# Optimization experiments

Measured on AMD Instinct MI355X. Metric: run time of the kernel, lower is better.

## Reference

```python
import jax, jax.numpy as jnp
import numpy as np

B, S, I, H = 64, 2048, 512, 512


def setup_inputs() -> dict:
    key = jax.random.key(0)
    k1, k2, k3 = jax.random.split(key, 3)
    x_enc = jax.random.normal(k1, (B, S, I), dtype=jnp.float32)
    # Packed gate weights: columns = [i | f | o | c | d], scaled like typical init
    W = jax.random.normal(k2, (I + H, 5 * H), dtype=jnp.float32) * (1.0 / np.sqrt(I + H))
    b = jax.random.normal(k3, (5 * H,), dtype=jnp.float32) * 0.01
    return {"x_enc": x_enc, "W": W, "b": b}


def reference(x_enc, W, b):
    Bb, Ss, Ii = x_enc.shape
    Hh = W.shape[1] // 5

    def step(carry, x_t):
        h, c = carry
        z = jnp.concatenate([x_t, h], axis=-1) @ W + b  # [B, 5H]
        zi, zf, zo, zc, zd = jnp.split(z, 5, axis=-1)
        i_t = jax.nn.sigmoid(zi)
        f_t = jax.nn.sigmoid(zf)
        o_t = jax.nn.sigmoid(zo)
        c_prime = f_t * c + i_t * jnp.tanh(zc)
        d_t = jnp.tanh(zd)
        c_new = c_prime + d_t * (c_prime - c)  # highway-style update
        h_new = o_t * jnp.tanh(c_new)
        return (h_new, c_new), h_new

    h0 = jnp.zeros((Bb, Hh), dtype=x_enc.dtype)
    c0 = jnp.zeros((Bb, Hh), dtype=x_enc.dtype)
    xs = jnp.transpose(x_enc, (1, 0, 2))  # [S, B, I]
    _, ys = jax.lax.scan(step, (h0, c0), xs)
    return jnp.transpose(ys, (1, 0, 2))  # [B, S, H]
```

## Files before the change

kernel.cpp:

```cpp
#include <hip/hip_runtime.h>
#include <stdint.h>


typedef _Float16 h8 __attribute__((ext_vector_type(8)));
typedef _Float16 h4v __attribute__((ext_vector_type(4)));
typedef float f4 __attribute__((ext_vector_type(4)));

#define SCOPE_AGENT __HIP_MEMORY_SCOPE_AGENT

__device__ __forceinline__ float sigf(float x) {
  x = fminf(fmaxf(x, -40.f), 40.f);
  return 1.f / (1.f + __expf(-x));
}
__device__ __forceinline__ float tanh_f(float x) {
  x = fminf(fmaxf(x, -20.f), 20.f);
  const float e = __expf(2.f * x);
  return (e - 1.f) / (e + 1.f);
}

__global__ __launch_bounds__(256) void k_wt(const float* __restrict__ W,
                                            _Float16* __restrict__ Wt) {
  __shared__ __align__(16) _Float16 tl[64][68];
  const int bk = blockIdx.x & 15;
  const int bn = blockIdx.x >> 4;
  const int t = threadIdx.x;
  {
    const int r = t >> 2, c4 = t & 3;
    const float4* s4 = (const float4*)(W + (size_t)(bk * 64 + r) * 2560 + bn * 64 + c4 * 16);
#pragma unroll
    for (int i = 0; i < 4; i++) {
      float4 v = s4[i];
      tl[r][c4 * 16 + i * 4 + 0] = (_Float16)v.x;
      tl[r][c4 * 16 + i * 4 + 1] = (_Float16)v.y;
      tl[r][c4 * 16 + i * 4 + 2] = (_Float16)v.z;
      tl[r][c4 * 16 + i * 4 + 3] = (_Float16)v.w;
    }
  }
  __syncthreads();
  {
    const int nr = t >> 2, kk = (t & 3) * 16;
    h8 o0, o1;
#pragma unroll
    for (int i = 0; i < 8; i++) {
      o0[i] = tl[kk + i][nr];
      o1[i] = tl[kk + 8 + i][nr];
    }
    _Float16* dst = Wt + (size_t)(bn * 64 + nr) * 1024 + bk * 64 + kk;
    *(h8*)dst = o0;
    *(h8*)(dst + 8) = o1;
  }
}

__global__ __launch_bounds__(256) void k_zx(const float* __restrict__ X,
                                            const _Float16* __restrict__ Wt,
                                            const float* __restrict__ bias,
                                            _Float16* __restrict__ Zx,
                                            int s_base, int CS) {
  __shared__ __align__(16) _Float16 As[128][72];
  __shared__ __align__(16) _Float16 Bs[128][72];
  const int bid = blockIdx.x;
  const int nblk = bid % 20;
  const int mblk = bid / 20;
  const int tilesPerB = CS >> 7;
  const int b = mblk / tilesPerB;
  const int s0 = (mblk - b * tilesPerB) << 7;
  const int t = threadIdx.x;
  const int wid = t >> 6, lane = t & 63;
  const int wr = wid >> 1, wc = wid & 1;
  const int lr = (lane >> 4) * 4, lc = lane & 15;
  const int koff = (lane >> 4) * 8;

  const f4 zero4 = {0.f, 0.f, 0.f, 0.f};
  f4 acc[4][4];
#pragma unroll
  for (int i = 0; i < 4; i++)
#pragma unroll
    for (int j = 0; j < 4; j++) acc[i][j] = zero4;

  const float* Xb = X + ((size_t)b * 2048 + (size_t)(s_base + s0)) * 512;
  const _Float16* Bb = Wt + (size_t)nblk * 128 * 1024;
  const int rA = t >> 1, hf = t & 1;

  for (int k0 = 0; k0 < 512; k0 += 64) {
    const float4* s4 = (const float4*)(Xb + (size_t)rA * 512 + k0 + hf * 32);
#pragma unroll
    for (int i = 0; i < 8; i++) {
      float4 v = s4[i];
      h4v o = {(_Float16)v.x, (_Float16)v.y, (_Float16)v.z, (_Float16)v.w};
      *(h4v*)&As[rA][hf * 32 + i * 4] = o;
    }
    const h8* bs = (const h8*)(Bb + (size_t)rA * 1024 + k0 + hf * 32);
#pragma unroll
    for (int i = 0; i < 4; i++) *(h8*)&Bs[rA][hf * 32 + i * 8] = bs[i];
    __syncthreads();
#pragma unroll
    for (int kk = 0; kk < 2; kk++) {
      h8 af[4], bf[4];
      const int kr = kk * 32 + koff;
#pragma unroll
      for (int i = 0; i < 4; i++) af[i] = *(const h8*)&As[wr * 64 + i * 16 + lc][kr];
#pragma unroll
      for (int j = 0; j < 4; j++) bf[j] = *(const h8*)&Bs[wc * 64 + j * 16 + lc][kr];
#pragma unroll
      for (int i = 0; i < 4; i++)
#pragma unroll
        for (int j = 0; j < 4; j++)
          acc[i][j] = __builtin_amdgcn_mfma_f32_16x16x32_f16(af[i], bf[j], acc[i][j], 0, 0, 0);
    }
    __syncthreads();
  }
#pragma unroll
  for (int j = 0; j < 4; j++) {
    const int col = nblk * 128 + wc * 64 + j * 16 + lc;
    const float bc = bias[col];
#pragma unroll
    for (int i = 0; i < 4; i++) {
#pragma unroll
      for (int r = 0; r < 4; r++) {
        const int srow = s0 + wr * 64 + i * 16 + lr + r;
        Zx[((size_t)b * CS + srow) * 2560 + col] = (_Float16)(acc[i][j][r] + bc);
      }
    }
  }
}

__global__ __launch_bounds__(256) void k_rec(
    const _Float16* __restrict__ Zx, const _Float16* __restrict__ Wt,
    float* __restrict__ Y, uint32_t* __restrict__ hbuf,
    _Float16* __restrict__ hstate, float* __restrict__ cstate,
    uint32_t* __restrict__ flags, int s_base, int CS) {
  __shared__ __align__(16) _Float16 WsT[40][520];
  __shared__ __align__(16) _Float16 hs[16][520];
  __shared__ __align__(16) float zsh[16][40];
  __shared__ __align__(16) _Float16 zxs[16][40];
  __shared__ __align__(16) float cbuf[128];
  __shared__ __align__(16) uint16_t hn[128];

  const int bid = blockIdx.x;
  const int grp = bid >> 6, ci = bid & 63;
  const int tid = threadIdx.x;
  const int wid = tid >> 6, lane = tid & 63;
  const int hbase = ci * 8;

#pragma unroll
  for (int i = 0; i < 10; i++) {
    const int idx = i * 256 + tid;
    const int lcw = idx >> 6;
    const int ch = idx & 63;
    const int g = lcw >> 3, j = lcw & 7;
    const h8* src = (const h8*)(Wt + (size_t)(g * 512 + hbase + j) * 1024 + 512 + ch * 8);
    *(h8*)&WsT[lcw][ch * 8] = *src;
  }
  if (tid < 128) {
    cbuf[tid] = cstate[(grp * 64 + ci) * 128 + tid];
    const int m = tid >> 3, j = tid & 7;
    _Float16 hv = hstate[(size_t)(grp * 16 + m) * 512 + hbase + j];
    hn[tid] = *(const uint16_t*)&hv;
  }
  __syncthreads();
  if (wid == 0) {
    const int m = lane >> 2, q = lane & 3;
    const uint32_t v = ((const uint32_t*)hn)[lane];
    __hip_atomic_store(&hbuf[(size_t)((0 * 4 + grp) * 16 + m) * 256 + ci * 4 + q], v,
                       __ATOMIC_RELAXED, SCOPE_AGENT);
    asm volatile("s_waitcnt vmcnt(0)" ::: "memory");
    if (lane == 0)
      __hip_atomic_store(&flags[grp * 64 + ci], 1u, __ATOMIC_RELAXED, SCOPE_AGENT);
  }

  uint32_t* hs32 = (uint32_t*)&hs[0][0];

  for (int t = 0; t < CS; t++) {
    if (wid == 3) {
      for (int c = lane; c < 80; c += 64) {
        const int m = c / 5, g = c % 5;
        const h8* src =
            (const h8*)(Zx + ((size_t)(grp * 16 + m) * CS + t) * 2560 + g * 512 + hbase);
        *(h8*)&zxs[m][g * 8] = *src;
      }
    }
    if (wid == 0) {
      const uint32_t target = (uint32_t)(t + 1);
      while (true) {
        const uint32_t v =
            __hip_atomic_load(&flags[grp * 64 + lane], __ATOMIC_RELAXED, SCOPE_AGENT);
        if (__all((int)(v >= target))) break;
      }
    }
    __syncthreads();
    {
      const uint32_t* src = hbuf + (size_t)(((t & 1) * 4 + grp) * 16) * 256;
#pragma unroll
      for (int i = 0; i < 16; i++) {
        const uint32_t v =
            __hip_atomic_load(&src[i * 256 + tid], __ATOMIC_RELAXED, SCOPE_AGENT);
        hs32[i * 260 + tid] = v;
      }
    }
    __syncthreads();
    if (wid < 3) {
      f4 acc = {0.f, 0.f, 0.f, 0.f};
      const int nloc = wid * 16 + (lane & 15);
      const int wrow = nloc < 40 ? nloc : 39;
      const int koff = (lane >> 4) * 8;
#pragma unroll
      for (int ks = 0; ks < 16; ks++) {
        const h8 a = *(const h8*)&hs[lane & 15][ks * 32 + koff];
        const h8 bb = *(const h8*)&WsT[wrow][ks * 32 + koff];
        acc = __builtin_amdgcn_mfma_f32_16x16x32_f16(a, bb, acc, 0, 0, 0);
      }
      if (nloc < 40) {
        const int rb = (lane >> 4) * 4;
#pragma unroll
        for (int r = 0; r < 4; r++)
          zsh[rb + r][nloc] = acc[r] + (float)zxs[rb + r][nloc];
      }
    }
    __syncthreads();
    if (tid < 128) {
      const int m = tid >> 3, j = tid & 7;
      const float zi = zsh[m][j], zf = zsh[m][8 + j], zo = zsh[m][16 + j];
      const float zc = zsh[m][24 + j], zd = zsh[m][32 + j];
      const float ig = sigf(zi), fg = sigf(zf), og = sigf(zo);
      const float c0 = cbuf[tid];
      const float cp = fg * c0 + ig * tanh_f(zc);
      const float dg = tanh_f(zd);
      const float cn = cp + dg * (cp - c0);
      const float hv = og * tanh_f(cn);
      cbuf[tid] = cn;
      Y[((size_t)(grp * 16 + m) * 2048 + (size_t)(s_base + t)) * 512 + hbase + j] = hv;
      const _Float16 hfv = (_Float16)hv;
      hn[tid] = *(const uint16_t*)&hfv;
      if (t == CS - 1) {
        cstate[(grp * 64 + ci) * 128 + tid] = cn;
        hstate[(size_t)(grp * 16 + m) * 512 + hbase + j] = hfv;
      }
    }
    __syncthreads();
    if (wid == 0) {
      const int m = lane >> 2, q = lane & 3;
      const uint32_t v = ((const uint32_t*)hn)[lane];
      __hip_atomic_store(
          &hbuf[(size_t)((((t + 1) & 1) * 4 + grp) * 16 + m) * 256 + ci * 4 + q], v,
          __ATOMIC_RELAXED, SCOPE_AGENT);
      asm volatile("s_waitcnt vmcnt(0)" ::: "memory");
      if (lane == 0)
        __hip_atomic_store(&flags[grp * 64 + ci], (uint32_t)(t + 2), __ATOMIC_RELAXED,
                           SCOPE_AGENT);
    }
  }
}

extern "C" void kernel_launch(void* const* d_in, const int* in_sizes, int n_in,
                              void* d_out, int out_size, void* d_ws, size_t ws_size,
                              hipStream_t stream) {
  const float* X = (const float*)d_in[0];
  const float* W = (const float*)d_in[1];
  const float* bias = (const float*)d_in[2];
  float* Y = (float*)d_out;
  char* ws = (char*)d_ws;

  const size_t szWt = (size_t)2560 * 1024 * 2;
  int CS = 128;
  for (int c = 2048; c >= 128; c >>= 1) {
    const size_t need = szWt + (size_t)64 * c * 2560 * 2 + 400 * 1024;
    if (need <= ws_size) { CS = c; break; }
  }
  const size_t offZx = szWt;
  const size_t szZx = (size_t)64 * CS * 2560 * 2;
  const size_t offHbuf = offZx + szZx;
  const size_t szHbuf = (size_t)2 * 4 * 16 * 256 * 4;
  const size_t offHst = offHbuf + szHbuf;
  const size_t szHst = (size_t)4 * 16 * 512 * 2;
  const size_t offCst = offHst + szHst;
  const size_t szCst = (size_t)4 * 64 * 128 * 4;
  const size_t offFlg = offCst + szCst;
  const size_t szFlg = 256 * 4;

  _Float16* Wt = (_Float16*)(ws + 0);
  _Float16* Zx = (_Float16*)(ws + offZx);
  uint32_t* hbuf = (uint32_t*)(ws + offHbuf);
  _Float16* hstate = (_Float16*)(ws + offHst);
  float* cstate = (float*)(ws + offCst);
  uint32_t* flags = (uint32_t*)(ws + offFlg);

  k_wt<<<640, 256, 0, stream>>>(W, Wt);
  (void)hipMemsetAsync(ws + offHst, 0, szHst + szCst, stream);

  const int nch = 2048 / CS;
  for (int ch = 0; ch < nch; ch++) {
    const int sb = ch * CS;
    k_zx<<<CS * 10, 256, 0, stream>>>(X, Wt, bias, Zx, sb, CS);
    (void)hipMemsetAsync(ws + offFlg, 0, szFlg, stream);
    k_rec<<<256, 256, 0, stream>>>(Zx, Wt, Y, hbuf, hstate, cstate, flags, sb, CS);
  }
  (void)in_sizes; (void)n_in; (void)out_size;
}
```

Baseline: 15.76 ms.

## Replace flag-based step barrier with tagged per-element h exchange

The separate per-block flag array and its polling wave are removed. Each h element is now stored with a 16-bit step tag in the upper half of a 32-bit word, and consumers spin on the tags of the data they load directly. This removes the extra syncthreads, the s_waitcnt before flag stores, and the flag memset between chunks. It also permutes block-to-column mapping, likely to spread blocks across XCDs. The hbuf doubles in size, and each element is published individually with a relaxed atomic, so ordering correctness depends on the tag check alone.

```diff
diff --git a/kernel.cpp b/kernel.cpp
--- a/kernel.cpp
+++ b/kernel.cpp
@@ -128,16 +128,16 @@
     const _Float16* __restrict__ Zx, const _Float16* __restrict__ Wt,
     float* __restrict__ Y, uint32_t* __restrict__ hbuf,
     _Float16* __restrict__ hstate, float* __restrict__ cstate,
-    uint32_t* __restrict__ flags, int s_base, int CS) {
+    int s_base, int CS) {
   __shared__ __align__(16) _Float16 WsT[40][520];
   __shared__ __align__(16) _Float16 hs[16][520];
   __shared__ __align__(16) float zsh[16][40];
   __shared__ __align__(16) _Float16 zxs[16][40];
   __shared__ __align__(16) float cbuf[128];
-  __shared__ __align__(16) uint16_t hn[128];
 
   const int bid = blockIdx.x;
-  const int grp = bid >> 6, ci = bid & 63;
+  const int grp = bid >> 6;
+  const int ci = ((bid & 7) << 3) | ((bid >> 3) & 7);
   const int tid = threadIdx.x;
   const int wid = tid >> 6, lane = tid & 63;
   const int hbase = ci * 8;
@@ -155,22 +155,19 @@
     cbuf[tid] = cstate[(grp * 64 + ci) * 128 + tid];
     const int m = tid >> 3, j = tid & 7;
     _Float16 hv = hstate[(size_t)(grp * 16 + m) * 512 + hbase + j];
-    hn[tid] = *(const uint16_t*)&hv;
+    uint16_t hb;
+    __builtin_memcpy(&hb, &hv, 2);
+    const uint32_t v = ((uint32_t)(s_base + 1) << 16) | (uint32_t)hb;
+    __hip_atomic_store(&hbuf[((size_t)((s_base & 1) * 4 + grp) * 16 + m) * 512 + hbase + j],
+                       v, __ATOMIC_RELAXED, SCOPE_AGENT);
   }
   __syncthreads();
-  if (wid == 0) {
-    const int m = lane >> 2, q = lane & 3;
-    const uint32_t v = ((const uint32_t*)hn)[lane];
-    __hip_atomic_store(&hbuf[(size_t)((0 * 4 + grp) * 16 + m) * 256 + ci * 4 + q], v,
-                       __ATOMIC_RELAXED, SCOPE_AGENT);
-    asm volatile("s_waitcnt vmcnt(0)" ::: "memory");
-    if (lane == 0)
-      __hip_atomic_store(&flags[grp * 64 + ci], 1u, __ATOMIC_RELAXED, SCOPE_AGENT);
-  }
 
   uint32_t* hs32 = (uint32_t*)&hs[0][0];
 
   for (int t = 0; t < CS; t++) {
+    const int G = s_base + t;
+    const uint32_t tag = (uint32_t)(G + 1);
     if (wid == 3) {
       for (int c = lane; c < 80; c += 64) {
         const int m = c / 5, g = c % 5;
@@ -179,22 +176,20 @@
         *(h8*)&zxs[m][g * 8] = *src;
       }
     }
-    if (wid == 0) {
-      const uint32_t target = (uint32_t)(t + 1);
-      while (true) {
-        const uint32_t v =
-            __hip_atomic_load(&flags[grp * 64 + lane], __ATOMIC_RELAXED, SCOPE_AGENT);
-        if (__all((int)(v >= target))) break;
-      }
-    }
-    __syncthreads();
     {
-      const uint32_t* src = hbuf + (size_t)(((t & 1) * 4 + grp) * 16) * 256;
+      const uint64_t* src =
+          (const uint64_t*)(hbuf + (size_t)((G & 1) * 4 + grp) * 16 * 512);
+      uint64_t w[16];
+#pragma unroll
+      for (int i = 0; i < 16; i++)
+        w[i] = __hip_atomic_load(&src[i * 256 + tid], __ATOMIC_RELAXED, SCOPE_AGENT);
 #pragma unroll
       for (int i = 0; i < 16; i++) {
-        const uint32_t v =
-            __hip_atomic_load(&src[i * 256 + tid], __ATOMIC_RELAXED, SCOPE_AGENT);
-        hs32[i * 260 + tid] = v;
+        while ((((uint32_t)w[i] >> 16) != tag) |
+               (((uint32_t)(w[i] >> 48)) != tag))
+          w[i] = __hip_atomic_load(&src[i * 256 + tid], __ATOMIC_RELAXED, SCOPE_AGENT);
+        hs32[i * 260 + tid] =
+            ((uint32_t)w[i] & 0xffffu) | (((uint32_t)(w[i] >> 32) & 0xffffu) << 16);
       }
     }
     __syncthreads();
@@ -228,25 +223,19 @@
       const float cn = cp + dg * (cp - c0);
       const float hv = og * tanh_f(cn);
       cbuf[tid] = cn;
-      Y[((size_t)(grp * 16 + m) * 2048 + (size_t)(s_base + t)) * 512 + hbase + j] = hv;
       const _Float16 hfv = (_Float16)hv;
-      hn[tid] = *(const uint16_t*)&hfv;
+      uint16_t hb;
+      __builtin_memcpy(&hb, &hfv, 2);
+      const uint32_t v = ((uint32_t)(G + 2) << 16) | (uint32_t)hb;
+      __hip_atomic_store(
+          &hbuf[((size_t)(((G + 1) & 1) * 4 + grp) * 16 + m) * 512 + hbase + j], v,
+          __ATOMIC_RELAXED, SCOPE_AGENT);
+      asm volatile("" ::: "memory");
+      Y[((size_t)(grp * 16 + m) * 2048 + (size_t)G) * 512 + hbase + j] = hv;
       if (t == CS - 1) {
         cstate[(grp * 64 + ci) * 128 + tid] = cn;
         hstate[(size_t)(grp * 16 + m) * 512 + hbase + j] = hfv;
       }
-    }
-    __syncthreads();
-    if (wid == 0) {
-      const int m = lane >> 2, q = lane & 3;
-      const uint32_t v = ((const uint32_t*)hn)[lane];
-      __hip_atomic_store(
-          &hbuf[(size_t)((((t + 1) & 1) * 4 + grp) * 16 + m) * 256 + ci * 4 + q], v,
-          __ATOMIC_RELAXED, SCOPE_AGENT);
-      asm volatile("s_waitcnt vmcnt(0)" ::: "memory");
-      if (lane == 0)
-        __hip_atomic_store(&flags[grp * 64 + ci], (uint32_t)(t + 2), __ATOMIC_RELAXED,
-                           SCOPE_AGENT);
     }
   }
 }
@@ -263,36 +252,32 @@
   const size_t szWt = (size_t)2560 * 1024 * 2;
   int CS = 128;
   for (int c = 2048; c >= 128; c >>= 1) {
-    const size_t need = szWt + (size_t)64 * c * 2560 * 2 + 400 * 1024;
+    const size_t need = szWt + (size_t)64 * c * 2560 * 2 + 512 * 1024;
     if (need <= ws_size) { CS = c; break; }
   }
   const size_t offZx = szWt;
   const size_t szZx = (size_t)64 * CS * 2560 * 2;
   const size_t offHbuf = offZx + szZx;
-  const size_t szHbuf = (size_t)2 * 4 * 16 * 256 * 4;
+  const size_t szHbuf = (size_t)2 * 4 * 16 * 512 * 4;
   const size_t offHst = offHbuf + szHbuf;
   const size_t szHst = (size_t)4 * 16 * 512 * 2;
   const size_t offCst = offHst + szHst;
   const size_t szCst = (size_t)4 * 64 * 128 * 4;
-  const size_t offFlg = offCst + szCst;
-  const size_t szFlg = 256 * 4;
 
   _Float16* Wt = (_Float16*)(ws + 0);
   _Float16* Zx = (_Float16*)(ws + offZx);
   uint32_t* hbuf = (uint32_t*)(ws + offHbuf);
   _Float16* hstate = (_Float16*)(ws + offHst);
   float* cstate = (float*)(ws + offCst);
-  uint32_t* flags = (uint32_t*)(ws + offFlg);
 
   k_wt<<<640, 256, 0, stream>>>(W, Wt);
-  (void)hipMemsetAsync(ws + offHst, 0, szHst + szCst, stream);
+  (void)hipMemsetAsync(ws + offHbuf, 0, szHbuf + szHst + szCst, stream);
 
   const int nch = 2048 / CS;
   for (int ch = 0; ch < nch; ch++) {
     const int sb = ch * CS;
     k_zx<<<CS * 10, 256, 0, stream>>>(X, Wt, bias, Zx, sb, CS);
-    (void)hipMemsetAsync(ws + offFlg, 0, szFlg, stream);
-    k_rec<<<256, 256, 0, stream>>>(Zx, Wt, Y, hbuf, hstate, cstate, flags, sb, CS);
+    k_rec<<<256, 256, 0, stream>>>(Zx, Wt, Y, hbuf, hstate, cstate, sb, CS);
   }
   (void)in_sizes; (void)n_in; (void)out_size;
 }
```

After: 13.91 ms. -11.7%, faster.
